# Kernel tuning notes

Hardware: AMD Instinct MI355X
Metric: run time of the kernel (lower is better)

Reference implementation:

```python
import jax, jax.numpy as jnp
import numpy as np

N = 100000      # nodes
E = 1600000     # directed edges (avg degree 16)
D_IN, D_H, D_OUT = 128, 128, 64


def glorot(k, fi, fo):
    s = (6.0 / (fi + fo)) ** 0.5
    return jax.random.uniform(k, (fi, fo), jnp.float32, -s, s)


def setup_inputs() -> dict:
    key = jax.random.key(0)
    ks = jax.random.split(key, 5)
    edges = jax.random.randint(ks[0], (2, E), 0, N)
    features = jax.random.normal(ks[1], (N, D_IN), dtype=jnp.float32)
    return dict(
        edges=edges,
        features=features,
        W0=glorot(ks[2], D_IN, D_H), b0=jnp.zeros((D_H,), jnp.float32),
        W1=glorot(ks[3], D_H, D_H), b1=jnp.zeros((D_H,), jnp.float32),
        W2=glorot(ks[4], D_H, D_OUT), b2=jnp.zeros((D_OUT,), jnp.float32),
    )


def _prep(edges):
    # add self-loops and compute symmetric GCN normalization D^-1/2 A_hat D^-1/2
    loop = jnp.arange(N)
    row = jnp.concatenate([edges[0], loop])  # source
    col = jnp.concatenate([edges[1], loop])  # target
    deg = jax.ops.segment_sum(jnp.ones((row.shape[0],), jnp.float32), col, num_segments=N)
    dinv = jnp.where(deg > 0, jax.lax.rsqrt(deg), 0.0)
    norm = dinv[row] * dinv[col]             # per-edge coefficient
    return row, col, norm


def gcn_conv(x, row, col, norm, W, b):
    x = x @ W                                 # [N, out]
    msg = x[row] * norm[:, None]              # gather + scale, [E+N, out]
    return jax.ops.segment_sum(msg, col, num_segments=N) + b


def reference(edges, features, W0, b0, W1, b1, W2, b2):
    row, col, norm = _prep(edges)
    h = jax.nn.relu(gcn_conv(features, row, col, norm, W0, b0))
    h = jax.nn.relu(gcn_conv(h, row, col, norm, W1, b1))
    h = gcn_conv(h, row, col, norm, W2, b2)
    return jax.nn.log_softmax(h, axis=1)
```

## Files before the change

kernel.cpp:

```cpp
#include <hip/hip_runtime.h>
#include <hip/hip_fp16.h>
#include <math.h>

#define NN 100000
#define EE 1600000
#define NB2 782
#define BN 128
#define NPART 512
#define CAP 2560

typedef __attribute__((ext_vector_type(8))) _Float16 half8;
typedef __attribute__((ext_vector_type(4))) float f32x4;
typedef __attribute__((ext_vector_type(4))) unsigned int u32x4;

__device__ inline unsigned short f2h(float x) {
    return __half_as_ushort(__float2half(x));
}
__device__ inline __half2 u2h2(unsigned u) {
    return __builtin_bit_cast(__half2, u);
}
__device__ inline unsigned h22u(__half2 h) {
    return __builtin_bit_cast(unsigned, h);
}


__global__ void prep_weights(const float* __restrict__ W0, const float* __restrict__ W1,
                             const float* __restrict__ W2, unsigned short* __restrict__ Wt0,
                             unsigned short* __restrict__ Wt1, unsigned short* __restrict__ Wt2,
                             int* __restrict__ bcount) {
    int g = blockIdx.x * 256 + threadIdx.x;
    if (g < NB2) bcount[g] = 0;
    if (g < 16384) {
        int n = g >> 7, k = g & 127;
        Wt0[g] = f2h(W0[k * 128 + n]);
    } else if (g < 32768) {
        int i = g - 16384;
        int n = i >> 7, k = i & 127;
        Wt1[i] = f2h(W1[k * 128 + n]);
    } else if (g < 40960) {
        int i = g - 32768;
        int n = i >> 7, k = i & 127;
        Wt2[i] = f2h(W2[k * 64 + n]);
    }
}


__global__ __launch_bounds__(256) void scatter_bump(const int* __restrict__ src,
                                                    const int* __restrict__ dst,
                                                    int* __restrict__ bcount,
                                                    int* __restrict__ P, int e) {
    __shared__ int cnt[NB2];
    __shared__ int basep[NB2];
    __shared__ int cur[NB2];
    int t = threadIdx.x;
    for (int i = t; i < NB2; i += 256) { cnt[i] = 0; cur[i] = 0; }
    __syncthreads();
    int chunk = (e + NPART - 1) / NPART;
    int b0 = blockIdx.x * chunk, b1 = min(e, b0 + chunk);
    for (int i = b0 + t; i < b1; i += 256)
        atomicAdd(&cnt[dst[i] >> 7], 1);
    __syncthreads();
    for (int i = t; i < NB2; i += 256) {
        int c = cnt[i];
        basep[i] = c ? atomicAdd(&bcount[i], c) : 0;
    }
    __syncthreads();
    for (int i = b0 + t; i < b1; i += 256) {
        int d = dst[i];
        int b = d >> 7;
        int p = basep[b] + atomicAdd(&cur[b], 1);
        P[(size_t)b * CAP + p] = (src[i] << 7) | (d & 127);
    }
}

__global__ __launch_bounds__(256) void bucket_build(const int* __restrict__ P,
                                                    const int* __restrict__ bcount,
                                                    int2* __restrict__ offs2,
                                                    float* __restrict__ dinv,
                                                    int* __restrict__ csr, int n) {
    __shared__ int cnt[BN];
    __shared__ int sc[BN];
    __shared__ int cur[BN];
    __shared__ int stage[CAP];
    int b = blockIdx.x, t = threadIdx.x;
    int base = b * CAP;
    int count = bcount[b];
    if (t < BN) cnt[t] = 0;
    __syncthreads();
    for (int i = t; i < count; i += 256)
        atomicAdd(&cnt[P[base + i] & 127], 1);
    __syncthreads();
    int v = 0;
    if (t < BN) {
        v = cnt[t];
        sc[t] = v;
    }
    for (int d = 1; d < BN; d <<= 1) {
        __syncthreads();
        int x = (t < BN && t >= d) ? sc[t - d] : 0;
        __syncthreads();
        if (t < BN) sc[t] += x;
    }
    __syncthreads();
    if (t < BN) {
        int myoff = sc[t] - v;
        int node = b * BN + t;
        if (node < n) {
            offs2[node] = make_int2(base + myoff, base + myoff + v);
            dinv[node] = 1.0f / sqrtf((float)(v + 1));
        }
        cur[t] = myoff;
    }
    __syncthreads();
    for (int i = t; i < count; i += 256) {
        int pe = P[base + i];
        int p = atomicAdd(&cur[pe & 127], 1);
        stage[p] = ((unsigned)pe) >> 7;
    }
    __syncthreads();
    for (int i = t; i < count; i += 256) csr[base + i] = stage[i];
}

template <bool F32>
__device__ inline half8 load_xrow(const void* A, int row, int col, int nrows) {
    if (row >= nrows) {
        u32x4 z = {0u, 0u, 0u, 0u};
        return __builtin_bit_cast(half8, z);
    }
    if (F32) {
        const float* p = (const float*)A + (size_t)row * 128 + col;
        float4 v0 = *(const float4*)p;
        float4 v1 = *(const float4*)(p + 4);
        u32x4 u;
        u.x = h22u(__floats2half2_rn(v0.x, v0.y));
        u.y = h22u(__floats2half2_rn(v0.z, v0.w));
        u.z = h22u(__floats2half2_rn(v1.x, v1.y));
        u.w = h22u(__floats2half2_rn(v1.z, v1.w));
        return __builtin_bit_cast(half8, u);
    } else {
        const unsigned short* p = (const unsigned short*)A + (size_t)row * 128 + col;
        u32x4 u = *(const u32x4*)p;
        return __builtin_bit_cast(half8, u);
    }
}

template <int DOUT, bool A_IS_F32>
__global__ __launch_bounds__(256) void gemm_mfma(const void* __restrict__ Aptr,
                                                 const unsigned short* __restrict__ Wt,
                                                 const float* __restrict__ dinv,
                                                 unsigned short* __restrict__ Y, int nrows) {
    constexpr int KP = 136;
    constexpr int NT = DOUT / 16;
    __shared__ unsigned short sB[DOUT * KP];
    const int row0 = blockIdx.x * 128;
    const int tid = threadIdx.x;

    for (int i = tid; i < DOUT * 16; i += 256) {
        int n = i >> 4, c = (i & 15) * 8;
        uint4 v = *(const uint4*)(Wt + n * 128 + c);
        *(uint4*)(&sB[n * KP + c]) = v;
    }
    __syncthreads();

    const int wave = tid >> 6;
    const int lane = tid & 63;
    const int m0 = lane & 15;
    const int kq = (lane >> 4) * 8;
    const int xr0 = row0 + wave * 32 + m0;
    const int xr1 = xr0 + 16;

    f32x4 acc[2][NT];
#pragma unroll
    for (int rt = 0; rt < 2; ++rt)
#pragma unroll
        for (int t = 0; t < NT; ++t) acc[rt][t] = (f32x4){0.f, 0.f, 0.f, 0.f};

#pragma unroll
    for (int k0 = 0; k0 < 128; k0 += 32) {
        half8 b0 = load_xrow<A_IS_F32>(Aptr, xr0, k0 + kq, nrows);
        half8 b1 = load_xrow<A_IS_F32>(Aptr, xr1, k0 + kq, nrows);
#pragma unroll
        for (int t = 0; t < NT; ++t) {
            half8 aW = *(const half8*)(&sB[(t * 16 + m0) * KP + k0 + kq]);
            acc[0][t] = __builtin_amdgcn_mfma_f32_16x16x32_f16(aW, b0, acc[0][t], 0, 0, 0);
            acc[1][t] = __builtin_amdgcn_mfma_f32_16x16x32_f16(aW, b1, acc[1][t], 0, 0, 0);
        }
    }

#pragma unroll
    for (int rt = 0; rt < 2; ++rt) {
        int xrow = row0 + wave * 32 + rt * 16 + m0;
        if (xrow < nrows) {
            float dv = dinv[xrow];
#pragma unroll
            for (int t = 0; t < NT; ++t) {
                uint2 o;
                o.x = h22u(__floats2half2_rn(acc[rt][t][0] * dv, acc[rt][t][1] * dv));
                o.y = h22u(__floats2half2_rn(acc[rt][t][2] * dv, acc[rt][t][3] * dv));
                *(uint2*)(Y + (size_t)xrow * DOUT + t * 16 + (lane >> 4) * 4) = o;
            }
        }
    }
}

__global__ __launch_bounds__(256) void agg128_f16(const unsigned short* __restrict__ Xp,
                                                  const int* __restrict__ csr,
                                                  const int2* __restrict__ offs2,
                                                  const float* __restrict__ dinv,
                                                  const float* __restrict__ bias,
                                                  unsigned short* __restrict__ Y, int n) {
    __shared__ int sIdx[4][64];
    int wv = threadIdx.x >> 6;
    int node = blockIdx.x * 4 + wv;
    if (node >= n) return;
    int lane = threadIdx.x & 63;
    int q = lane >> 4;
    int l = lane & 15;
    int2 se = offs2[node];
    int s = se.x, deg = se.y - se.x;
    if (lane < deg) sIdx[wv][lane] = csr[s + lane];
    int dcap = min(deg, 64);
    const int* idx = sIdx[wv];
    const __half2 hz = __floats2half2_rn(0.f, 0.f);
    __half2 aA0 = hz, aA1 = hz, aA2 = hz, aA3 = hz;
    __half2 aB0 = hz, aB1 = hz, aB2 = hz, aB3 = hz;
    int j = q;
    for (; j + 12 < dcap; j += 16) {
        int s0 = idx[j], s1 = idx[j + 4], s2 = idx[j + 8], s3 = idx[j + 12];
        uint4 u0 = *(const uint4*)(Xp + (size_t)s0 * 128 + l * 8);
        uint4 u1 = *(const uint4*)(Xp + (size_t)s1 * 128 + l * 8);
        uint4 u2 = *(const uint4*)(Xp + (size_t)s2 * 128 + l * 8);
        uint4 u3 = *(const uint4*)(Xp + (size_t)s3 * 128 + l * 8);
        aA0 = __hadd2(aA0, u2h2(u0.x)); aA1 = __hadd2(aA1, u2h2(u0.y));
        aA2 = __hadd2(aA2, u2h2(u0.z)); aA3 = __hadd2(aA3, u2h2(u0.w));
        aB0 = __hadd2(aB0, u2h2(u1.x)); aB1 = __hadd2(aB1, u2h2(u1.y));
        aB2 = __hadd2(aB2, u2h2(u1.z)); aB3 = __hadd2(aB3, u2h2(u1.w));
        aA0 = __hadd2(aA0, u2h2(u2.x)); aA1 = __hadd2(aA1, u2h2(u2.y));
        aA2 = __hadd2(aA2, u2h2(u2.z)); aA3 = __hadd2(aA3, u2h2(u2.w));
        aB0 = __hadd2(aB0, u2h2(u3.x)); aB1 = __hadd2(aB1, u2h2(u3.y));
        aB2 = __hadd2(aB2, u2h2(u3.z)); aB3 = __hadd2(aB3, u2h2(u3.w));
    }
    for (; j < dcap; j += 4) {
        int s0 = idx[j];
        uint4 u = *(const uint4*)(Xp + (size_t)s0 * 128 + l * 8);
        aA0 = __hadd2(aA0, u2h2(u.x)); aA1 = __hadd2(aA1, u2h2(u.y));
        aA2 = __hadd2(aA2, u2h2(u.z)); aA3 = __hadd2(aA3, u2h2(u.w));
    }
    for (int p = s + 64 + q; p < s + deg; p += 4) {
        int s0 = csr[p];
        uint4 u = *(const uint4*)(Xp + (size_t)s0 * 128 + l * 8);
        aB0 = __hadd2(aB0, u2h2(u.x)); aB1 = __hadd2(aB1, u2h2(u.y));
        aB2 = __hadd2(aB2, u2h2(u.z)); aB3 = __hadd2(aB3, u2h2(u.w));
    }
    if (q == 0) {
        uint4 u = *(const uint4*)(Xp + (size_t)node * 128 + l * 8);
        aB0 = __hadd2(aB0, u2h2(u.x)); aB1 = __hadd2(aB1, u2h2(u.y));
        aB2 = __hadd2(aB2, u2h2(u.z)); aB3 = __hadd2(aB3, u2h2(u.w));
    }
    float2 fA, fB;
    fA = __half22float2(aA0); fB = __half22float2(aB0);
    float r0 = fA.x + fB.x, r1 = fA.y + fB.y;
    fA = __half22float2(aA1); fB = __half22float2(aB1);
    float r2 = fA.x + fB.x, r3 = fA.y + fB.y;
    fA = __half22float2(aA2); fB = __half22float2(aB2);
    float r4 = fA.x + fB.x, r5 = fA.y + fB.y;
    fA = __half22float2(aA3); fB = __half22float2(aB3);
    float r6 = fA.x + fB.x, r7 = fA.y + fB.y;
    r0 += __shfl_xor(r0, 16); r0 += __shfl_xor(r0, 32);
    r1 += __shfl_xor(r1, 16); r1 += __shfl_xor(r1, 32);
    r2 += __shfl_xor(r2, 16); r2 += __shfl_xor(r2, 32);
    r3 += __shfl_xor(r3, 16); r3 += __shfl_xor(r3, 32);
    r4 += __shfl_xor(r4, 16); r4 += __shfl_xor(r4, 32);
    r5 += __shfl_xor(r5, 16); r5 += __shfl_xor(r5, 32);
    r6 += __shfl_xor(r6, 16); r6 += __shfl_xor(r6, 32);
    r7 += __shfl_xor(r7, 16); r7 += __shfl_xor(r7, 32);
    if (q == 0) {
        float di = dinv[node];
        float4 bA = *(const float4*)(bias + l * 8);
        float4 bB = *(const float4*)(bias + l * 8 + 4);
        r0 = fmaxf(fmaf(di, r0, bA.x), 0.f); r1 = fmaxf(fmaf(di, r1, bA.y), 0.f);
        r2 = fmaxf(fmaf(di, r2, bA.z), 0.f); r3 = fmaxf(fmaf(di, r3, bA.w), 0.f);
        r4 = fmaxf(fmaf(di, r4, bB.x), 0.f); r5 = fmaxf(fmaf(di, r5, bB.y), 0.f);
        r6 = fmaxf(fmaf(di, r6, bB.z), 0.f); r7 = fmaxf(fmaf(di, r7, bB.w), 0.f);
        uint4 o;
        o.x = h22u(__floats2half2_rn(r0, r1));
        o.y = h22u(__floats2half2_rn(r2, r3));
        o.z = h22u(__floats2half2_rn(r4, r5));
        o.w = h22u(__floats2half2_rn(r6, r7));
        *(uint4*)(Y + (size_t)node * 128 + l * 8) = o;
    }
}

__global__ __launch_bounds__(256) void agg_softmax64_f16(const unsigned short* __restrict__ Xp,
                                                         const int* __restrict__ csr,
                                                         const int2* __restrict__ offs2,
                                                         const float* __restrict__ dinv,
                                                         const float* __restrict__ bias,
                                                         float* __restrict__ out, int n) {
    __shared__ int sIdx[4][64];
    int wv = threadIdx.x >> 6;
    int node = blockIdx.x * 4 + wv;
    if (node >= n) return;
    int lane = threadIdx.x & 63;
    int g8 = lane >> 3;
    int l = lane & 7;
    int2 se = offs2[node];
    int s = se.x, deg = se.y - se.x;
    if (lane < deg) sIdx[wv][lane] = csr[s + lane];
    int dcap = min(deg, 64);
    const int* idx = sIdx[wv];
    const __half2 hz = __floats2half2_rn(0.f, 0.f);
    __half2 aA0 = hz, aA1 = hz, aA2 = hz, aA3 = hz;
    __half2 aB0 = hz, aB1 = hz, aB2 = hz, aB3 = hz;
    int j = g8;
    for (; j + 8 < dcap; j += 16) {
        int s0 = idx[j], s1 = idx[j + 8];
        uint4 u0 = *(const uint4*)(Xp + (size_t)s0 * 64 + l * 8);
        uint4 u1 = *(const uint4*)(Xp + (size_t)s1 * 64 + l * 8);
        aA0 = __hadd2(aA0, u2h2(u0.x)); aA1 = __hadd2(aA1, u2h2(u0.y));
        aA2 = __hadd2(aA2, u2h2(u0.z)); aA3 = __hadd2(aA3, u2h2(u0.w));
        aB0 = __hadd2(aB0, u2h2(u1.x)); aB1 = __hadd2(aB1, u2h2(u1.y));
        aB2 = __hadd2(aB2, u2h2(u1.z)); aB3 = __hadd2(aB3, u2h2(u1.w));
    }
    if (j < dcap) {
        int s0 = idx[j];
        uint4 u = *(const uint4*)(Xp + (size_t)s0 * 64 + l * 8);
        aA0 = __hadd2(aA0, u2h2(u.x)); aA1 = __hadd2(aA1, u2h2(u.y));
        aA2 = __hadd2(aA2, u2h2(u.z)); aA3 = __hadd2(aA3, u2h2(u.w));
    }
    for (int p = s + 64 + g8; p < s + deg; p += 8) {
        int s0 = csr[p];
        uint4 u = *(const uint4*)(Xp + (size_t)s0 * 64 + l * 8);
        aB0 = __hadd2(aB0, u2h2(u.x)); aB1 = __hadd2(aB1, u2h2(u.y));
        aB2 = __hadd2(aB2, u2h2(u.z)); aB3 = __hadd2(aB3, u2h2(u.w));
    }
    if (g8 == 0) {
        uint4 u = *(const uint4*)(Xp + (size_t)node * 64 + l * 8);
        aB0 = __hadd2(aB0, u2h2(u.x)); aB1 = __hadd2(aB1, u2h2(u.y));
        aB2 = __hadd2(aB2, u2h2(u.z)); aB3 = __hadd2(aB3, u2h2(u.w));
    }
    float2 fA, fB;
    fA = __half22float2(aA0); fB = __half22float2(aB0);
    float r0 = fA.x + fB.x, r1 = fA.y + fB.y;
    fA = __half22float2(aA1); fB = __half22float2(aB1);
    float r2 = fA.x + fB.x, r3 = fA.y + fB.y;
    fA = __half22float2(aA2); fB = __half22float2(aB2);
    float r4 = fA.x + fB.x, r5 = fA.y + fB.y;
    fA = __half22float2(aA3); fB = __half22float2(aB3);
    float r6 = fA.x + fB.x, r7 = fA.y + fB.y;
    r0 += __shfl_xor(r0, 8); r0 += __shfl_xor(r0, 16); r0 += __shfl_xor(r0, 32);
    r1 += __shfl_xor(r1, 8); r1 += __shfl_xor(r1, 16); r1 += __shfl_xor(r1, 32);
    r2 += __shfl_xor(r2, 8); r2 += __shfl_xor(r2, 16); r2 += __shfl_xor(r2, 32);
    r3 += __shfl_xor(r3, 8); r3 += __shfl_xor(r3, 16); r3 += __shfl_xor(r3, 32);
    r4 += __shfl_xor(r4, 8); r4 += __shfl_xor(r4, 16); r4 += __shfl_xor(r4, 32);
    r5 += __shfl_xor(r5, 8); r5 += __shfl_xor(r5, 16); r5 += __shfl_xor(r5, 32);
    r6 += __shfl_xor(r6, 8); r6 += __shfl_xor(r6, 16); r6 += __shfl_xor(r6, 32);
    r7 += __shfl_xor(r7, 8); r7 += __shfl_xor(r7, 16); r7 += __shfl_xor(r7, 32);
    if (g8 == 0) {
        float di = dinv[node];
        float4 bA = *(const float4*)(bias + l * 8);
        float4 bB = *(const float4*)(bias + l * 8 + 4);
        r0 = fmaf(di, r0, bA.x); r1 = fmaf(di, r1, bA.y);
        r2 = fmaf(di, r2, bA.z); r3 = fmaf(di, r3, bA.w);
        r4 = fmaf(di, r4, bB.x); r5 = fmaf(di, r5, bB.y);
        r6 = fmaf(di, r6, bB.z); r7 = fmaf(di, r7, bB.w);
        float m = fmaxf(fmaxf(fmaxf(r0, r1), fmaxf(r2, r3)), fmaxf(fmaxf(r4, r5), fmaxf(r6, r7)));
#pragma unroll
        for (int o = 4; o > 0; o >>= 1) m = fmaxf(m, __shfl_xor(m, o));
        float ssum = __expf(r0 - m) + __expf(r1 - m) + __expf(r2 - m) + __expf(r3 - m) +
                     __expf(r4 - m) + __expf(r5 - m) + __expf(r6 - m) + __expf(r7 - m);
#pragma unroll
        for (int o = 4; o > 0; o >>= 1) ssum += __shfl_xor(ssum, o);
        float lg = m + __logf(ssum);
        float4 o0 = make_float4(r0 - lg, r1 - lg, r2 - lg, r3 - lg);
        float4 o1 = make_float4(r4 - lg, r5 - lg, r6 - lg, r7 - lg);
        *(float4*)(out + (size_t)node * 64 + l * 8) = o0;
        *(float4*)(out + (size_t)node * 64 + l * 8 + 4) = o1;
    }
}


extern "C" void kernel_launch(void* const* d_in, const int* in_sizes, int n_in,
                              void* d_out, int out_size, void* d_ws, size_t ws_size,
                              hipStream_t stream) {
    const int* edges = (const int*)d_in[0];
    const float* feat = (const float*)d_in[1];
    const float* W0 = (const float*)d_in[2];
    const float* b0 = (const float*)d_in[3];
    const float* W1 = (const float*)d_in[4];
    const float* b1 = (const float*)d_in[5];
    const float* W2 = (const float*)d_in[6];
    const float* b2 = (const float*)d_in[7];

    const int N = NN;
    const int E = EE;

    char* ws = (char*)d_ws;
    int* bcount = (int*)ws;
    int2* offs2 = (int2*)(bcount + ((NB2 + 1) & ~1));
    float* dinv = (float*)(offs2 + N);
    int* P = (int*)(dinv + N);
    int* csr = P + (size_t)NB2 * CAP;
    unsigned short* Wt0 = (unsigned short*)(csr + (size_t)NB2 * CAP);
    unsigned short* Wt1 = Wt0 + 16384;
    unsigned short* Wt2 = Wt1 + 16384;
    size_t off = (size_t)((char*)(Wt2 + 8192) - ws);
    off = (off + 255) & ~(size_t)255;
    unsigned short* bufA = (unsigned short*)(ws + off);
    unsigned short* bufB = bufA + (size_t)N * 128;

    const int* esrc = edges;
    const int* edst = edges + E;

    prep_weights<<<160, 256, 0, stream>>>(W0, W1, W2, Wt0, Wt1, Wt2, bcount);
    scatter_bump<<<NPART, 256, 0, stream>>>(esrc, edst, bcount, P, E);
    bucket_build<<<NB2, 256, 0, stream>>>(P, bcount, offs2, dinv, csr, N);

    const int gemmBlocks = (N + 127) / 128;
    const int aggBlocks = (N + 3) / 4;

    gemm_mfma<128, true><<<gemmBlocks, 256, 0, stream>>>(feat, Wt0, dinv, bufA, N);
    agg128_f16<<<aggBlocks, 256, 0, stream>>>(bufA, csr, offs2, dinv, b0, bufB, N);
    gemm_mfma<128, false><<<gemmBlocks, 256, 0, stream>>>(bufB, Wt1, dinv, bufA, N);
    agg128_f16<<<aggBlocks, 256, 0, stream>>>(bufA, csr, offs2, dinv, b1, bufB, N);
    gemm_mfma<64, false><<<gemmBlocks, 256, 0, stream>>>(bufB, Wt2, dinv, bufA, N);
    agg_softmax64_f16<<<aggBlocks, 256, 0, stream>>>(bufA, csr, offs2, dinv, b2, (float*)d_out, N);
}
```

Before: 372.0 us.

## Assign one 16-lane group per node in 128-wide aggregation kernel

Restructures agg128_f16 so each node is handled by 16 lanes instead of a full 64-lane wavefront, giving 16 nodes per block. Each group walks its whole neighbor list, reading indices straight from global CSR, so the shared-memory index staging and the cross-quarter shuffle reduction go away. Every lane now writes output rather than only one quarter of the wave. The cost is less memory-level parallelism per node and more divergence between high- and low-degree nodes that share a wavefront.

```diff
diff --git a/kernel.cpp b/kernel.cpp
--- a/kernel.cpp
+++ b/kernel.cpp
@@ -209,54 +209,47 @@
                                                   const float* __restrict__ dinv,
                                                   const float* __restrict__ bias,
                                                   unsigned short* __restrict__ Y, int n) {
-    __shared__ int sIdx[4][64];
-    int wv = threadIdx.x >> 6;
-    int node = blockIdx.x * 4 + wv;
+    const int tid = threadIdx.x;
+    const int node = blockIdx.x * 16 + (tid >> 4);
     if (node >= n) return;
-    int lane = threadIdx.x & 63;
-    int q = lane >> 4;
-    int l = lane & 15;
+    const int l = tid & 15;
+    const unsigned short* __restrict__ Xl = Xp + l * 8;
+
     int2 se = offs2[node];
     int s = se.x, deg = se.y - se.x;
-    if (lane < deg) sIdx[wv][lane] = csr[s + lane];
-    int dcap = min(deg, 64);
-    const int* idx = sIdx[wv];
     const __half2 hz = __floats2half2_rn(0.f, 0.f);
     __half2 aA0 = hz, aA1 = hz, aA2 = hz, aA3 = hz;
     __half2 aB0 = hz, aB1 = hz, aB2 = hz, aB3 = hz;
-    int j = q;
-    for (; j + 12 < dcap; j += 16) {
-        int s0 = idx[j], s1 = idx[j + 4], s2 = idx[j + 8], s3 = idx[j + 12];
-        uint4 u0 = *(const uint4*)(Xp + (size_t)s0 * 128 + l * 8);
-        uint4 u1 = *(const uint4*)(Xp + (size_t)s1 * 128 + l * 8);
-        uint4 u2 = *(const uint4*)(Xp + (size_t)s2 * 128 + l * 8);
-        uint4 u3 = *(const uint4*)(Xp + (size_t)s3 * 128 + l * 8);
+    int j = 0;
+    for (; j + 4 <= deg; j += 4) {
+        int i0 = csr[s + j], i1 = csr[s + j + 1], i2 = csr[s + j + 2], i3 = csr[s + j + 3];
+        uint4 u0 = *(const uint4*)(Xl + (size_t)i0 * 128);
+        uint4 u1 = *(const uint4*)(Xl + (size_t)i1 * 128);
+        uint4 u2 = *(const uint4*)(Xl + (size_t)i2 * 128);
+        uint4 u3 = *(const uint4*)(Xl + (size_t)i3 * 128);
         aA0 = __hadd2(aA0, u2h2(u0.x)); aA1 = __hadd2(aA1, u2h2(u0.y));
         aA2 = __hadd2(aA2, u2h2(u0.z)); aA3 = __hadd2(aA3, u2h2(u0.w));
-        aB0 = __hadd2(aB0, u2h2(u1.x)); aB1 = __hadd2(aB1, u2h2(u1.y));
-        aB2 = __hadd2(aB2, u2h2(u1.z)); aB3 = __hadd2(aB3, u2h2(u1.w));
-        aA0 = __hadd2(aA0, u2h2(u2.x)); aA1 = __hadd2(aA1, u2h2(u2.y));
-        aA2 = __hadd2(aA2, u2h2(u2.z)); aA3 = __hadd2(aA3, u2h2(u2.w));
+        aB0 = __hadd2(aB0, u2h2(u2.x)); aB1 = __hadd2(aB1, u2h2(u2.y));
+        aB2 = __hadd2(aB2, u2h2(u2.z)); aB3 = __hadd2(aB3, u2h2(u2.w));
+        aA0 = __hadd2(aA0, u2h2(u1.x)); aA1 = __hadd2(aA1, u2h2(u1.y));
+        aA2 = __hadd2(aA2, u2h2(u1.z)); aA3 = __hadd2(aA3, u2h2(u1.w));
         aB0 = __hadd2(aB0, u2h2(u3.x)); aB1 = __hadd2(aB1, u2h2(u3.y));
         aB2 = __hadd2(aB2, u2h2(u3.z)); aB3 = __hadd2(aB3, u2h2(u3.w));
     }
-    for (; j < dcap; j += 4) {
-        int s0 = idx[j];
-        uint4 u = *(const uint4*)(Xp + (size_t)s0 * 128 + l * 8);
+    for (; j < deg; ++j) {
+        int i0 = csr[s + j];
+        uint4 u = *(const uint4*)(Xl + (size_t)i0 * 128);
         aA0 = __hadd2(aA0, u2h2(u.x)); aA1 = __hadd2(aA1, u2h2(u.y));
         aA2 = __hadd2(aA2, u2h2(u.z)); aA3 = __hadd2(aA3, u2h2(u.w));
     }
-    for (int p = s + 64 + q; p < s + deg; p += 4) {
-        int s0 = csr[p];
-        uint4 u = *(const uint4*)(Xp + (size_t)s0 * 128 + l * 8);
+    {
+        uint4 u = *(const uint4*)(Xl + (size_t)node * 128);
         aB0 = __hadd2(aB0, u2h2(u.x)); aB1 = __hadd2(aB1, u2h2(u.y));
         aB2 = __hadd2(aB2, u2h2(u.z)); aB3 = __hadd2(aB3, u2h2(u.w));
     }
-    if (q == 0) {
-        uint4 u = *(const uint4*)(Xp + (size_t)node * 128 + l * 8);
-        aB0 = __hadd2(aB0, u2h2(u.x)); aB1 = __hadd2(aB1, u2h2(u.y));
-        aB2 = __hadd2(aB2, u2h2(u.z)); aB3 = __hadd2(aB3, u2h2(u.w));
-    }
+    float di = dinv[node];
+    float4 bA = *(const float4*)(bias + l * 8);
+    float4 bB = *(const float4*)(bias + l * 8 + 4);
     float2 fA, fB;
     fA = __half22float2(aA0); fB = __half22float2(aB0);
     float r0 = fA.x + fB.x, r1 = fA.y + fB.y;
@@ -266,29 +259,16 @@
     float r4 = fA.x + fB.x, r5 = fA.y + fB.y;
     fA = __half22float2(aA3); fB = __half22float2(aB3);
     float r6 = fA.x + fB.x, r7 = fA.y + fB.y;
-    r0 += __shfl_xor(r0, 16); r0 += __shfl_xor(r0, 32);
-    r1 += __shfl_xor(r1, 16); r1 += __shfl_xor(r1, 32);
-    r2 += __shfl_xor(r2, 16); r2 += __shfl_xor(r2, 32);
-    r3 += __shfl_xor(r3, 16); r3 += __shfl_xor(r3, 32);
-    r4 += __shfl_xor(r4, 16); r4 += __shfl_xor(r4, 32);
-    r5 += __shfl_xor(r5, 16); r5 += __shfl_xor(r5, 32);
-    r6 += __shfl_xor(r6, 16); r6 += __shfl_xor(r6, 32);
-    r7 += __shfl_xor(r7, 16); r7 += __shfl_xor(r7, 32);
-    if (q == 0) {
-        float di = dinv[node];
-        float4 bA = *(const float4*)(bias + l * 8);
-        float4 bB = *(const float4*)(bias + l * 8 + 4);
-        r0 = fmaxf(fmaf(di, r0, bA.x), 0.f); r1 = fmaxf(fmaf(di, r1, bA.y), 0.f);
-        r2 = fmaxf(fmaf(di, r2, bA.z), 0.f); r3 = fmaxf(fmaf(di, r3, bA.w), 0.f);
-        r4 = fmaxf(fmaf(di, r4, bB.x), 0.f); r5 = fmaxf(fmaf(di, r5, bB.y), 0.f);
-        r6 = fmaxf(fmaf(di, r6, bB.z), 0.f); r7 = fmaxf(fmaf(di, r7, bB.w), 0.f);
-        uint4 o;
-        o.x = h22u(__floats2half2_rn(r0, r1));
-        o.y = h22u(__floats2half2_rn(r2, r3));
-        o.z = h22u(__floats2half2_rn(r4, r5));
-        o.w = h22u(__floats2half2_rn(r6, r7));
-        *(uint4*)(Y + (size_t)node * 128 + l * 8) = o;
-    }
+    r0 = fmaxf(fmaf(di, r0, bA.x), 0.f); r1 = fmaxf(fmaf(di, r1, bA.y), 0.f);
+    r2 = fmaxf(fmaf(di, r2, bA.z), 0.f); r3 = fmaxf(fmaf(di, r3, bA.w), 0.f);
+    r4 = fmaxf(fmaf(di, r4, bB.x), 0.f); r5 = fmaxf(fmaf(di, r5, bB.y), 0.f);
+    r6 = fmaxf(fmaf(di, r6, bB.z), 0.f); r7 = fmaxf(fmaf(di, r7, bB.w), 0.f);
+    uint4 o;
+    o.x = h22u(__floats2half2_rn(r0, r1));
+    o.y = h22u(__floats2half2_rn(r2, r3));
+    o.z = h22u(__floats2half2_rn(r4, r5));
+    o.w = h22u(__floats2half2_rn(r6, r7));
+    *(uint4*)(Y + (size_t)node * 128 + l * 8) = o;
 }
 
 __global__ __launch_bounds__(256) void agg_softmax64_f16(const unsigned short* __restrict__ Xp,
@@ -417,12 +397,13 @@
     bucket_build<<<NB2, 256, 0, stream>>>(P, bcount, offs2, dinv, csr, N);
 
     const int gemmBlocks = (N + 127) / 128;
+    const int agg128Blocks = (N + 15) / 16;
     const int aggBlocks = (N + 3) / 4;
 
     gemm_mfma<128, true><<<gemmBlocks, 256, 0, stream>>>(feat, Wt0, dinv, bufA, N);
-    agg128_f16<<<aggBlocks, 256, 0, stream>>>(bufA, csr, offs2, dinv, b0, bufB, N);
+    agg128_f16<<<agg128Blocks, 256, 0, stream>>>(bufA, csr, offs2, dinv, b0, bufB, N);
     gemm_mfma<128, false><<<gemmBlocks, 256, 0, stream>>>(bufB, Wt1, dinv, bufA, N);
-    agg128_f16<<<aggBlocks, 256, 0, stream>>>(bufA, csr, offs2, dinv, b1, bufB, N);
+    agg128_f16<<<agg128Blocks, 256, 0, stream>>>(bufA, csr, offs2, dinv, b1, bufB, N);
     gemm_mfma<64, false><<<gemmBlocks, 256, 0, stream>>>(bufB, Wt2, dinv, bufA, N);
     agg_softmax64_f16<<<aggBlocks, 256, 0, stream>>>(bufA, csr, offs2, dinv, b2, (float*)d_out, N);
 }
```

After: 369.3 us. Within noise of the previous version (-0.7%).
